# Kernel tuning notes

Hardware: AMD Instinct MI355X
Metric: run time of the kernel (lower is better)

Reference implementation:

```python
import jax, jax.numpy as jnp
import numpy as np

B, T_DIM, N, D, HID, NH = 2, 512, 6, 32, 128, 4
HD = HID // NH  # 32
GH = max(32, D)  # gater hidden = 32
FD = 128  # final_dim
EPS = 1e-5


def _ln(x, w, b):
    mu = jnp.mean(x, axis=-1, keepdims=True)
    var = jnp.var(x, axis=-1, keepdims=True)
    return (x - mu) * jax.lax.rsqrt(var + EPS) * w + b


def setup_inputs() -> dict:
    key = jax.random.key(0)
    ks = jax.random.split(key, 16)
    s_d = 1.0 / np.sqrt(D)
    s_h = 1.0 / np.sqrt(HID)
    s_g = 1.0 / np.sqrt(GH)
    return {
        "per_t_forces": jax.random.normal(ks[0], (B, T_DIM, N, D), jnp.float32),
        # gater: LayerNorm(D) -> Linear(D,GH) -> SiLU -> Linear(GH,1) (bias zero-init)
        "g_ln_w": jnp.ones((D,), jnp.float32),
        "g_ln_b": jnp.zeros((D,), jnp.float32),
        "g_w1": jax.random.uniform(ks[1], (D, GH), jnp.float32, -s_d, s_d),
        "g_b1": jax.random.uniform(ks[2], (GH,), jnp.float32, -s_d, s_d),
        "g_w2": jax.random.uniform(ks[3], (GH, 1), jnp.float32, -s_g, s_g),
        "g_b2": jnp.zeros((1,), jnp.float32),
        # QKV / out projections
        "q_w": jax.random.uniform(ks[4], (D, HID), jnp.float32, -s_d, s_d),
        "q_b": jax.random.uniform(ks[5], (HID,), jnp.float32, -s_d, s_d),
        "k_w": jax.random.uniform(ks[6], (D, HID), jnp.float32, -s_d, s_d),
        "k_b": jax.random.uniform(ks[7], (HID,), jnp.float32, -s_d, s_d),
        "v_w": jax.random.uniform(ks[8], (D, HID), jnp.float32, -s_d, s_d),
        "v_b": jax.random.uniform(ks[9], (HID,), jnp.float32, -s_d, s_d),
        "o_w": jax.random.uniform(ks[10], (HID, HID), jnp.float32, -s_h, s_h),
        "o_b": jax.random.uniform(ks[11], (HID,), jnp.float32, -s_h, s_h),
        # final: LayerNorm(HID) -> Linear(HID,FD) -> SiLU
        "f_ln_w": jnp.ones((HID,), jnp.float32),
        "f_ln_b": jnp.zeros((HID,), jnp.float32),
        "f_w": jax.random.uniform(ks[12], (HID, FD), jnp.float32, -s_h, s_h),
        "f_b": jax.random.uniform(ks[13], (FD,), jnp.float32, -s_h, s_h),
        "T": T_DIM,
    }


def reference(per_t_forces, g_ln_w, g_ln_b, g_w1, g_b1, g_w2, g_b2,
              q_w, q_b, k_w, k_b, v_w, v_b, o_w, o_b,
              f_ln_w, f_ln_b, f_w, f_b, T):
    b, tt, n, d = per_t_forces.shape
    L = T * n
    x = per_t_forces.reshape(b, L, d)

    # per-force learned gating
    h = jax.nn.silu(_ln(x, g_ln_w, g_ln_b) @ g_w1 + g_b1)
    gates = jax.nn.sigmoid((h @ g_w2 + g_b2)[..., 0])  # [B, L]
    g = gates[..., None]

    # gated QKV
    Q = (x @ q_w + q_b) * g
    K = (x @ k_w + k_b) * g
    V = (x @ v_w + v_b) * g

    Qh = Q.reshape(b, L, NH, HD)
    Kh = K.reshape(b, L, NH, HD)
    Vh = V.reshape(b, L, NH, HD)

    scale = 1.0 / np.sqrt(HD)
    scores = jnp.einsum("bihd,bjhd->bhij", Qh, Kh) * scale  # [B,NH,L,L]

    # block-causal over time: token j masked out if its time block > time of i
    t_idx = jnp.arange(L) // n
    mask = t_idx[None, :] > t_idx[:, None]  # [L, L], True = masked
    scores = jnp.where(mask[None, None], -jnp.inf, scores)

    A = jnp.maximum(jax.nn.softmax(scores, axis=-1), 1e-9)
    attn = jnp.einsum("bhij,bjhd->bihd", A, Vh).reshape(b, L, HID)

    out = attn @ o_w + o_b                     # [B, L, HID]
    per_t = out.reshape(b, T, n, HID).mean(axis=2)  # mean-pool over forces
    final = jax.nn.silu(_ln(per_t, f_ln_w, f_ln_b) @ f_w + f_b)  # [B, T, FD]
    return final
```

## Files before the change

kernel.cpp:

```cpp
#include <hip/hip_runtime.h>
#include <hip/hip_bf16.h>

#define BB   2
#define TT   512
#define NF   6
#define DD   32
#define HIDD 128
#define NHH  4
#define HDD  32
#define GHH  32
#define FDD  128
#define LL   (TT*NF)
#define EPSF 1e-5f
#define NQT16 (LL/16)

typedef __attribute__((ext_vector_type(8))) short  bf16x8;
typedef __attribute__((ext_vector_type(4))) float  f32x4;

#define MFMA16x16x32(a,b,c) __builtin_amdgcn_mfma_f32_16x16x32_bf16(a,b,c,0,0,0)

__device__ __forceinline__ unsigned short bfh(float f) {
    union { __hip_bfloat16 b; unsigned short u; } cv;
    cv.b = __float2bfloat16(f);
    return cv.u;
}
__device__ __forceinline__ float bff(unsigned short u) {
    return __uint_as_float(((unsigned)u) << 16);
}
__device__ __forceinline__ unsigned pk_bf16(float a, float b) {
    union { __hip_bfloat162 h2; unsigned u; } cv;
    cv.h2 = __float22bfloat162_rn(make_float2(a, b));
    return cv.u;
}
__device__ __forceinline__ bf16x8 ld8(const unsigned short* p) {
    return *reinterpret_cast<const bf16x8*>(p);
}

__device__ __forceinline__ float fexp2(float x) {
#if __has_builtin(__builtin_amdgcn_exp2f)
    return __builtin_amdgcn_exp2f(x);
#else
    return exp2f(x);
#endif
}

struct Frags {
    bf16x8 k0, k1;
    bf16x8 k2, k3;
    bf16x8 v0, v1, v2, v3;
};

__device__ __forceinline__ void load_tile(
    const unsigned short* __restrict__ Kh,
    const unsigned short* __restrict__ Vth,
    size_t hbT, int j0, int kloc0, int kloc1, int quad,
    size_t vb0, size_t vb1, Frags& f)
{
    const size_t kX0 = (hbT + j0 + kloc0) * HDD + quad * 8;
    const size_t kX1 = (hbT + j0 + kloc1) * HDD + quad * 8;
    f.k0 = ld8(Kh + kX0);
    f.k1 = ld8(Kh + kX1);
    f.k2 = ld8(Kh + kX0 + (size_t)32 * HDD);
    f.k3 = ld8(Kh + kX1 + (size_t)32 * HDD);
    const size_t vX = (size_t)j0 + quad * 8, vY = vX + 32;
    f.v0 = ld8(Vth + vb0 + vX);
    f.v1 = ld8(Vth + vb1 + vX);
    f.v2 = ld8(Vth + vb0 + vY);
    f.v3 = ld8(Vth + vb1 + vY);
}

__device__ __forceinline__ void compute_tile(
    const Frags& f, const bf16x8 qfh, const bf16x8 qfl,
    int j0, int jminw, int jend, int quad,
    float& m, float& l, f32x4& o0, f32x4& o1)
{
    const f32x4 z = {0.f, 0.f, 0.f, 0.f};
    f32x4 s0 = MFMA16x16x32(f.k0, qfh, z);
    f32x4 s1 = MFMA16x16x32(f.k1, qfh, z);
    f32x4 s2 = MFMA16x16x32(f.k2, qfh, z);
    f32x4 s3 = MFMA16x16x32(f.k3, qfh, z);
    s0 = MFMA16x16x32(f.k0, qfl, s0);
    s1 = MFMA16x16x32(f.k1, qfl, s1);
    s2 = MFMA16x16x32(f.k2, qfl, s2);
    s3 = MFMA16x16x32(f.k3, qfl, s3);

    float e[16], mx, ls, corr;
    if (j0 + 64 <= jminw) {
        f32x4 m4 = s0;
        #pragma unroll
        for (int r2 = 0; r2 < 4; r2++)
            m4[r2] = fmaxf(fmaxf(m4[r2], s1[r2]), fmaxf(s2[r2], s3[r2]));
        mx = fmaxf(fmaxf(m4[0], m4[1]), fmaxf(m4[2], m4[3]));
        mx = fmaxf(mx, __shfl_xor(mx, 16));
        mx = fmaxf(mx, __shfl_xor(mx, 32));
        mx = fmaxf(m, mx);
        corr = fexp2(m - mx); m = mx;
        ls = 0.f;
        #pragma unroll
        for (int r2 = 0; r2 < 4; r2++) {
            float e0 = fexp2(s0[r2] - mx);
            float e1 = fexp2(s1[r2] - mx);
            float e2 = fexp2(s2[r2] - mx);
            float e3 = fexp2(s3[r2] - mx);
            e[r2] = e0; e[4 + r2] = e1; e[8 + r2] = e2; e[12 + r2] = e3;
            ls += (e0 + e1) + (e2 + e3);
        }
    } else {
        const int je = jend - j0;
        const int k0 = 8 * quad;
        float t[16];
        #pragma unroll
        for (int r2 = 0; r2 < 4; r2++) {
            t[r2]      = (k0 + r2          < je) ? s0[r2] : -1e30f;
            t[4 + r2]  = (k0 + 4 + r2      < je) ? s1[r2] : -1e30f;
            t[8 + r2]  = (32 + k0 + r2     < je) ? s2[r2] : -1e30f;
            t[12 + r2] = (32 + k0 + 4 + r2 < je) ? s3[r2] : -1e30f;
        }
        mx = t[0];
        #pragma unroll
        for (int i = 1; i < 16; i++) mx = fmaxf(mx, t[i]);
        mx = fmaxf(mx, __shfl_xor(mx, 16));
        mx = fmaxf(mx, __shfl_xor(mx, 32));
        mx = fmaxf(m, mx);
        corr = fexp2(m - mx); m = mx;
        ls = 0.f;
        #pragma unroll
        for (int r2 = 0; r2 < 4; r2++) {
            float e0 = fexp2(t[r2] - mx);
            float e1 = fexp2(t[4 + r2] - mx);
            float e2 = fexp2(t[8 + r2] - mx);
            float e3 = fexp2(t[12 + r2] - mx);
            e0 = (k0 + r2          < je) ? e0 : 0.f;
            e1 = (k0 + 4 + r2      < je) ? e1 : 0.f;
            e2 = (32 + k0 + r2     < je) ? e2 : 0.f;
            e3 = (32 + k0 + 4 + r2 < je) ? e3 : 0.f;
            e[r2] = e0; e[4 + r2] = e1; e[8 + r2] = e2; e[12 + r2] = e3;
            ls += (e0 + e1) + (e2 + e3);
        }
    }
    l = l * corr + ls;
    #pragma unroll
    for (int i = 0; i < 4; i++) { o0[i] *= corr; o1[i] *= corr; }

    union { unsigned u[4]; bf16x8 v; } pbX, pbY;
    pbX.u[0] = pk_bf16(e[0],  e[1]);
    pbX.u[1] = pk_bf16(e[2],  e[3]);
    pbX.u[2] = pk_bf16(e[4],  e[5]);
    pbX.u[3] = pk_bf16(e[6],  e[7]);
    pbY.u[0] = pk_bf16(e[8],  e[9]);
    pbY.u[1] = pk_bf16(e[10], e[11]);
    pbY.u[2] = pk_bf16(e[12], e[13]);
    pbY.u[3] = pk_bf16(e[14], e[15]);

    o0 = MFMA16x16x32(f.v0, pbX.v, o0);
    o1 = MFMA16x16x32(f.v1, pbX.v, o1);
    o0 = MFMA16x16x32(f.v2, pbY.v, o0);
    o1 = MFMA16x16x32(f.v3, pbY.v, o1);
}

__global__ __launch_bounds__(128) void gate_qkv_kernel(
    const float* __restrict__ x,
    const float* __restrict__ g_ln_w, const float* __restrict__ g_ln_b,
    const float* __restrict__ g_w1,   const float* __restrict__ g_b1,
    const float* __restrict__ g_w2,   const float* __restrict__ g_b2,
    const float* __restrict__ q_w,    const float* __restrict__ q_b,
    const float* __restrict__ k_w,    const float* __restrict__ k_b,
    const float* __restrict__ v_w,    const float* __restrict__ v_b,
    unsigned short* __restrict__ Qh, unsigned short* __restrict__ Ql,
    unsigned short* __restrict__ Kh,
    unsigned short* __restrict__ Vth)
{
    const int tok0 = blockIdx.x * 4;
    const int tid  = threadIdx.x;

    __shared__ float xs[4][DD];
    __shared__ float lns[4][DD];
    __shared__ float hs[4][GHH];
    __shared__ float gate_s[4];

    xs[tid >> 5][tid & 31] = x[(size_t)tok0 * DD + tid];
    __syncthreads();

    const int tk = (tid >> 5) & 1;
    const int d5 = tid & 31;
    if (tid < 64) {
        #pragma unroll
        for (int tt = 0; tt < 2; tt++) {
            int t = tt * 2 + tk;
            float xv = xs[t][d5];
            float s1 = xv, s2 = xv * xv;
            #pragma unroll
            for (int m = 16; m >= 1; m >>= 1) {
                s1 += __shfl_xor(s1, m, 32);
                s2 += __shfl_xor(s2, m, 32);
            }
            float mu  = s1 * (1.0f / DD);
            float var = s2 * (1.0f / DD) - mu * mu;
            float r   = rsqrtf(var + EPSF);
            lns[t][d5] = (xv - mu) * r * g_ln_w[d5] + g_ln_b[d5];
        }
    }
    __syncthreads();
    if (tid < 64) {
        #pragma unroll
        for (int tt = 0; tt < 2; tt++) {
            int t = tt * 2 + tk;
            float acc = g_b1[d5];
            #pragma unroll
            for (int d = 0; d < DD; d++) acc += lns[t][d] * g_w1[d * GHH + d5];
            hs[t][d5] = acc / (1.0f + __expf(-acc));
        }
    }
    __syncthreads();
    if (tid < 64) {
        #pragma unroll
        for (int tt = 0; tt < 2; tt++) {
            int t = tt * 2 + tk;
            float p = hs[t][d5] * g_w2[d5];
            #pragma unroll
            for (int m = 16; m >= 1; m >>= 1) p += __shfl_xor(p, m, 32);
            if (d5 == 0) gate_s[t] = 1.0f / (1.0f + __expf(-(p + g_b2[0])));
        }
    }
    __syncthreads();

    const int col = tid;
    float aq[4], ak[4], av[4];
    #pragma unroll
    for (int t = 0; t < 4; t++) { aq[t] = q_b[col]; ak[t] = k_b[col]; av[t] = v_b[col]; }
    #pragma unroll
    for (int d = 0; d < DD; d++) {
        float wq = q_w[d * HIDD + col];
        float wk = k_w[d * HIDD + col];
        float wv = v_w[d * HIDD + col];
        #pragma unroll
        for (int t = 0; t < 4; t++) {
            float xd = xs[t][d];
            aq[t] += xd * wq; ak[t] += xd * wk; av[t] += xd * wv;
        }
    }

    const int b    = tok0 / LL;
    const int l0   = tok0 - b * LL;
    const int head = col >> 5;
    const int d5c  = col & 31;
    const float scale = 0.25503486f;

    unsigned short vh[4];
    #pragma unroll
    for (int t = 0; t < 4; t++) {
        const float g = gate_s[t];
        const size_t a = ((size_t)(b * NHH + head) * LL + l0 + t) * HDD + d5c;
        float qv = aq[t] * g * scale;
        unsigned short h = bfh(qv); Qh[a] = h; Ql[a] = bfh(qv - bff(h));
        Kh[a] = bfh(ak[t] * g);
        vh[t] = bfh(av[t] * g);
    }
    const size_t vbase = ((size_t)(b * NHH + head) * HDD + d5c) * LL + l0;
    *(ushort4*)(Vth + vbase) = make_ushort4(vh[0], vh[1], vh[2], vh[3]);
}

__global__ __launch_bounds__(256) void attn_mfma(
    const unsigned short* __restrict__ Qh, const unsigned short* __restrict__ Ql,
    const unsigned short* __restrict__ Kh,
    const unsigned short* __restrict__ Vth,
    float* __restrict__ P, int C, int NCH)
{
    const int lin = blockIdx.x;
    const int bh  = lin & 7;
    const int jj  = lin >> 3;
    const int ch  = jj / (LL / 64);
    const int qt  = (LL / 64 - 1) - (jj % (LL / 64));
    const int j0c = C * ch;
    const int jmax_blk = ((qt * 64 + 63) / NF + 1) * NF;
    if (j0c >= jmax_blk) return;

    const int tid  = threadIdx.x;
    const int w    = tid >> 6;
    const int lane = tid & 63;
    const int rr   = lane & 15;
    const int quad = lane >> 4;

    const int ig0   = qt * 64 + w * 16;
    const int ig    = ig0 + rr;
    const int jend  = (ig / NF + 1) * NF;
    const int jmaxw = ((ig0 + 15) / NF + 1) * NF;
    const int jminw = (ig0 / NF + 1) * NF;

    const int kend = min(jmaxw - j0c, C);
    if (kend <= 0) return;

    const size_t hbT = (size_t)bh * LL;
    const size_t qo  = (hbT + ig) * HDD + quad * 8;
    const bf16x8 qfh = ld8(Qh + qo);
    const bf16x8 qfl = ld8(Ql + qo);

    const int kloc0 = 8 * (rr >> 2) + (rr & 3);
    const int kloc1 = kloc0 + 4;

    const size_t vb0 = ((size_t)bh * HDD + rr)      * LL;
    const size_t vb1 = ((size_t)bh * HDD + rr + 16) * LL;

    f32x4 oA0 = {0.f,0.f,0.f,0.f}, oA1 = {0.f,0.f,0.f,0.f};
    f32x4 oB0 = {0.f,0.f,0.f,0.f}, oB1 = {0.f,0.f,0.f,0.f};
    f32x4 oC0 = {0.f,0.f,0.f,0.f}, oC1 = {0.f,0.f,0.f,0.f};
    float mA = -1e30f, lA = 0.f, mB = -1e30f, lB = 0.f, mC = -1e30f, lC = 0.f;

    const int ntile = (kend + 63) >> 6;

    for (int i = 0; i < ntile; i += 3) {
        const int  j0A  = j0c + (i << 6);
        const bool hasB = (i + 1 < ntile);
        const bool hasC = (i + 2 < ntile);
        const int  j0B  = j0c + ((hasB ? i + 1 : i) << 6);
        const int  j0C  = j0c + ((hasC ? i + 2 : i) << 6);

        Frags fA, fB, fC;
        load_tile(Kh, Vth, hbT, j0A, kloc0, kloc1, quad, vb0, vb1, fA);
        load_tile(Kh, Vth, hbT, j0B, kloc0, kloc1, quad, vb0, vb1, fB);
        load_tile(Kh, Vth, hbT, j0C, kloc0, kloc1, quad, vb0, vb1, fC);

        compute_tile(fA, qfh, qfl, j0A, jminw, jend, quad, mA, lA, oA0, oA1);
        if (hasB)
            compute_tile(fB, qfh, qfl, j0B, jminw, jend, quad, mB, lB, oB0, oB1);
        if (hasC)
            compute_tile(fC, qfh, qfl, j0C, jminw, jend, quad, mC, lC, oC0, oC1);
    }

    const float mm = fmaxf(mA, fmaxf(mB, mC));
    const float wa = fexp2(mA - mm), wb = fexp2(mB - mm), wc = fexp2(mC - mm);
    float l = lA * wa + lB * wb + lC * wc;
    f32x4 o0, o1;
    #pragma unroll
    for (int i = 0; i < 4; i++) {
        o0[i] = oA0[i] * wa + oB0[i] * wb + oC0[i] * wc;
        o1[i] = oA1[i] * wa + oB1[i] * wb + oC1[i] * wc;
    }

    l += __shfl_xor(l, 16);
    l += __shfl_xor(l, 32);

    float* dst = P + ((((size_t)bh * NQT16 + (ig0 >> 4)) * NCH + ch) * 16 + rr) * 36;
    *(f32x4*)(dst + quad * 4)      = o0;
    *(f32x4*)(dst + 16 + quad * 4) = o1;
    if (quad == 0) { dst[32] = mm; dst[33] = l; }
}

__global__ __launch_bounds__(128) void final_kernel(
    const float* __restrict__ P,
    const float* __restrict__ o_w,    const float* __restrict__ o_b,
    const float* __restrict__ f_ln_w, const float* __restrict__ f_ln_b,
    const float* __restrict__ f_w,    const float* __restrict__ f_b,
    float* __restrict__ out, int C, int NCH)
{
    const int t = blockIdx.x;
    const int b = blockIdx.y;
    const int d = threadIdx.x;
    const int h  = d >> 5;
    const int hd = d & 31;
    const int bh = b * NHH + h;

    __shared__ float ms[HIDD];
    __shared__ float lnbuf[HIDD];
    __shared__ float w1[2], w2[2];

    const int jmax = (t + 1) * NF;
    const int nch  = min(NCH, (jmax + C - 1) / C);

    float M[NF], L[NF], O[NF];
    #pragma unroll
    for (int f = 0; f < NF; f++) { M[f] = -1e30f; L[f] = 0.f; O[f] = 0.f; }

    for (int c = 0; c < nch; c++) {
        #pragma unroll
        for (int f = 0; f < NF; f++) {
            const int row = t * NF + f;
            const float* pr = P + ((((size_t)bh * NQT16 + (row >> 4)) * NCH + c)
                                   * 16 + (row & 15)) * 36;
            const float mc = pr[32], lc = pr[33], oc = pr[hd];
            const float mm = fmaxf(M[f], mc);
            const float sa = fexp2(M[f] - mm), sb = fexp2(mc - mm);
            O[f] = O[f] * sa + oc * sb;
            L[f] = L[f] * sa + lc * sb;
            M[f] = mm;
        }
    }
    float acc = 0.0f;
    #pragma unroll
    for (int f = 0; f < NF; f++) acc += O[f] / L[f];
    acc *= (1.0f / NF);
    ms[d] = acc;
    __syncthreads();

    float ov = o_b[d];
    for (int k = 0; k < HIDD; k++) ov += ms[k] * o_w[k * HIDD + d];

    float s1 = ov, s2 = ov * ov;
    #pragma unroll
    for (int m = 32; m >= 1; m >>= 1) { s1 += __shfl_xor(s1, m); s2 += __shfl_xor(s2, m); }
    if ((d & 63) == 0) { w1[d >> 6] = s1; w2[d >> 6] = s2; }
    __syncthreads();
    float S1 = w1[0] + w1[1], S2 = w2[0] + w2[1];
    float mu  = S1 * (1.0f / HIDD);
    float var = S2 * (1.0f / HIDD) - mu * mu;
    float r   = rsqrtf(var + EPSF);
    float lnv = (ov - mu) * r * f_ln_w[d] + f_ln_b[d];
    lnbuf[d] = lnv;
    __syncthreads();

    float fv = f_b[d];
    for (int k = 0; k < HIDD; k++) fv += lnbuf[k] * f_w[k * HIDD + d];
    fv = fv / (1.0f + __expf(-fv));

    out[((size_t)(b * TT + t)) * FDD + d] = fv;
}

extern "C" void kernel_launch(void* const* d_in, const int* in_sizes, int n_in,
                              void* d_out, int out_size, void* d_ws, size_t ws_size,
                              hipStream_t stream)
{
    const float* x      = (const float*)d_in[0];
    const float* g_ln_w = (const float*)d_in[1];
    const float* g_ln_b = (const float*)d_in[2];
    const float* g_w1   = (const float*)d_in[3];
    const float* g_b1   = (const float*)d_in[4];
    const float* g_w2   = (const float*)d_in[5];
    const float* g_b2   = (const float*)d_in[6];
    const float* q_w    = (const float*)d_in[7];
    const float* q_b    = (const float*)d_in[8];
    const float* k_w    = (const float*)d_in[9];
    const float* k_b    = (const float*)d_in[10];
    const float* v_w    = (const float*)d_in[11];
    const float* v_b    = (const float*)d_in[12];
    const float* o_w    = (const float*)d_in[13];
    const float* o_b    = (const float*)d_in[14];
    const float* f_ln_w = (const float*)d_in[15];
    const float* f_ln_b = (const float*)d_in[16];
    const float* f_w    = (const float*)d_in[17];
    const float* f_b    = (const float*)d_in[18];

    const size_t ntok = (size_t)BB * NHH * LL * HDD;
    unsigned short* Qh  = (unsigned short*)d_ws;
    unsigned short* Ql  = Qh  + ntok;
    unsigned short* Kh  = Ql  + ntok;
    unsigned short* Vth = Kh + 2 * ntok;
    float* Pw = (float*)(Vth + 2 * ntok);

    const long long bf_floats = (long long)(6 * ntok) / 2;
    const long long unit = 8LL * NQT16 * 16 * 36;
    long long avail = (long long)(ws_size / 4) - bf_floats - 4096;
    int NCH = (int)(avail / unit);
    if (NCH > 16) NCH = 16;
    if (NCH < 1) NCH = 1;
    const int C = 64 * ((LL + 64 * NCH - 1) / (64 * NCH));

    gate_qkv_kernel<<<(BB * LL) / 4, 128, 0, stream>>>(
        x, g_ln_w, g_ln_b, g_w1, g_b1, g_w2, g_b2,
        q_w, q_b, k_w, k_b, v_w, v_b, Qh, Ql, Kh, Vth);

    attn_mfma<<<(LL / 64) * NCH * BB * NHH, 256, 0, stream>>>(
        Qh, Ql, Kh, Vth, Pw, C, NCH);

    final_kernel<<<dim3(TT, BB), 128, 0, stream>>>(
        Pw, o_w, o_b, f_ln_w, f_ln_b, f_w, f_b, (float*)d_out, C, NCH);
}
```

Measured before the change: 160.3 us.

## Stage K/V chunk in LDS and fix chunk count to eight

Each attention block now cooperatively copies its 384-key chunk of K and transposed V into shared memory (with row padding on V), then the four waves read MFMA fragments from LDS instead of global memory. The three-way independent online-softmax streams are replaced by a single stream with one-tile software prefetch from LDS. The chunk count is now hard-coded to 8 instead of being derived from workspace size. This cuts redundant global/L2 traffic across waves, at the cost of a barrier, about 48KB of LDS per block (lower occupancy), and less ILP in the softmax loop.

```diff
diff --git a/kernel.cpp b/kernel.cpp
--- a/kernel.cpp
+++ b/kernel.cpp
@@ -14,6 +14,10 @@
 #define EPSF 1e-5f
 #define NQT16 (LL/16)
 
+#define NCHC 8
+#define CCH  384
+#define VPAD 8
+
 typedef __attribute__((ext_vector_type(8))) short  bf16x8;
 typedef __attribute__((ext_vector_type(4))) float  f32x4;
 
@@ -50,23 +54,22 @@
     bf16x8 v0, v1, v2, v3;
 };
 
-__device__ __forceinline__ void load_tile(
-    const unsigned short* __restrict__ Kh,
-    const unsigned short* __restrict__ Vth,
-    size_t hbT, int j0, int kloc0, int kloc1, int quad,
-    size_t vb0, size_t vb1, Frags& f)
-{
-    const size_t kX0 = (hbT + j0 + kloc0) * HDD + quad * 8;
-    const size_t kX1 = (hbT + j0 + kloc1) * HDD + quad * 8;
-    f.k0 = ld8(Kh + kX0);
-    f.k1 = ld8(Kh + kX1);
-    f.k2 = ld8(Kh + kX0 + (size_t)32 * HDD);
-    f.k3 = ld8(Kh + kX1 + (size_t)32 * HDD);
-    const size_t vX = (size_t)j0 + quad * 8, vY = vX + 32;
-    f.v0 = ld8(Vth + vb0 + vX);
-    f.v1 = ld8(Vth + vb1 + vX);
-    f.v2 = ld8(Vth + vb0 + vY);
-    f.v3 = ld8(Vth + vb1 + vY);
+__device__ __forceinline__ void load_tile_lds(
+    const unsigned short* ldsK, const unsigned short* ldsV,
+    int j0loc, int kloc0, int kloc1, int quad, int rr, Frags& f)
+{
+    const int kX0 = (j0loc + kloc0) * HDD + quad * 8;
+    const int kX1 = (j0loc + kloc1) * HDD + quad * 8;
+    f.k0 = ld8(ldsK + kX0);
+    f.k1 = ld8(ldsK + kX1);
+    f.k2 = ld8(ldsK + kX0 + 32 * HDD);
+    f.k3 = ld8(ldsK + kX1 + 32 * HDD);
+    const int vX = j0loc + quad * 8, vY = vX + 32;
+    const int vr0 = rr * (CCH + VPAD), vr1 = (rr + 16) * (CCH + VPAD);
+    f.v0 = ld8(ldsV + vr0 + vX);
+    f.v1 = ld8(ldsV + vr1 + vX);
+    f.v2 = ld8(ldsV + vr0 + vY);
+    f.v3 = ld8(ldsV + vr1 + vY);
 }
 
 __device__ __forceinline__ void compute_tile(
@@ -264,18 +267,38 @@
     const unsigned short* __restrict__ Qh, const unsigned short* __restrict__ Ql,
     const unsigned short* __restrict__ Kh,
     const unsigned short* __restrict__ Vth,
-    float* __restrict__ P, int C, int NCH)
+    float* __restrict__ P)
 {
     const int lin = blockIdx.x;
     const int bh  = lin & 7;
     const int jj  = lin >> 3;
     const int ch  = jj / (LL / 64);
     const int qt  = (LL / 64 - 1) - (jj % (LL / 64));
-    const int j0c = C * ch;
+    const int j0c = CCH * ch;
     const int jmax_blk = ((qt * 64 + 63) / NF + 1) * NF;
     if (j0c >= jmax_blk) return;
 
-    const int tid  = threadIdx.x;
+    __shared__ __align__(16) unsigned short ldsK[CCH * HDD];
+    __shared__ __align__(16) unsigned short ldsV[HDD * (CCH + VPAD)];
+
+    const int tid = threadIdx.x;
+
+    {
+        const unsigned short* gK = Kh + ((size_t)bh * LL + j0c) * HDD;
+        const unsigned short* gV = Vth + (size_t)bh * HDD * LL + j0c;
+        const int r  = tid >> 3;
+        const int c8 = tid & 7;
+        #pragma unroll
+        for (int it = 0; it < CCH / 64; it++) {
+            const int uk = it * 256 + tid;
+            *reinterpret_cast<bf16x8*>(&ldsK[uk * 8]) = ld8(gK + uk * 8);
+            const int off = it * 64 + c8 * 8;
+            *reinterpret_cast<bf16x8*>(&ldsV[r * (CCH + VPAD) + off]) =
+                ld8(gV + (size_t)r * LL + off);
+        }
+    }
+    __syncthreads();
+
     const int w    = tid >> 6;
     const int lane = tid & 63;
     const int rr   = lane & 15;
@@ -287,63 +310,42 @@
     const int jmaxw = ((ig0 + 15) / NF + 1) * NF;
     const int jminw = (ig0 / NF + 1) * NF;
 
-    const int kend = min(jmaxw - j0c, C);
+    const int kend = min(jmaxw - j0c, CCH);
     if (kend <= 0) return;
 
-    const size_t hbT = (size_t)bh * LL;
-    const size_t qo  = (hbT + ig) * HDD + quad * 8;
+    const size_t qo = ((size_t)bh * LL + ig) * HDD + quad * 8;
     const bf16x8 qfh = ld8(Qh + qo);
     const bf16x8 qfl = ld8(Ql + qo);
 
     const int kloc0 = 8 * (rr >> 2) + (rr & 3);
     const int kloc1 = kloc0 + 4;
 
-    const size_t vb0 = ((size_t)bh * HDD + rr)      * LL;
-    const size_t vb1 = ((size_t)bh * HDD + rr + 16) * LL;
-
-    f32x4 oA0 = {0.f,0.f,0.f,0.f}, oA1 = {0.f,0.f,0.f,0.f};
-    f32x4 oB0 = {0.f,0.f,0.f,0.f}, oB1 = {0.f,0.f,0.f,0.f};
-    f32x4 oC0 = {0.f,0.f,0.f,0.f}, oC1 = {0.f,0.f,0.f,0.f};
-    float mA = -1e30f, lA = 0.f, mB = -1e30f, lB = 0.f, mC = -1e30f, lC = 0.f;
+    f32x4 o0 = {0.f,0.f,0.f,0.f}, o1 = {0.f,0.f,0.f,0.f};
+    float m = -1e30f, l = 0.f;
 
     const int ntile = (kend + 63) >> 6;
 
-    for (int i = 0; i < ntile; i += 3) {
-        const int  j0A  = j0c + (i << 6);
-        const bool hasB = (i + 1 < ntile);
-        const bool hasC = (i + 2 < ntile);
-        const int  j0B  = j0c + ((hasB ? i + 1 : i) << 6);
-        const int  j0C  = j0c + ((hasC ? i + 2 : i) << 6);
-
-        Frags fA, fB, fC;
-        load_tile(Kh, Vth, hbT, j0A, kloc0, kloc1, quad, vb0, vb1, fA);
-        load_tile(Kh, Vth, hbT, j0B, kloc0, kloc1, quad, vb0, vb1, fB);
-        load_tile(Kh, Vth, hbT, j0C, kloc0, kloc1, quad, vb0, vb1, fC);
-
-        compute_tile(fA, qfh, qfl, j0A, jminw, jend, quad, mA, lA, oA0, oA1);
-        if (hasB)
-            compute_tile(fB, qfh, qfl, j0B, jminw, jend, quad, mB, lB, oB0, oB1);
-        if (hasC)
-            compute_tile(fC, qfh, qfl, j0C, jminw, jend, quad, mC, lC, oC0, oC1);
-    }
-
-    const float mm = fmaxf(mA, fmaxf(mB, mC));
-    const float wa = fexp2(mA - mm), wb = fexp2(mB - mm), wc = fexp2(mC - mm);
-    float l = lA * wa + lB * wb + lC * wc;
-    f32x4 o0, o1;
-    #pragma unroll
-    for (int i = 0; i < 4; i++) {
-        o0[i] = oA0[i] * wa + oB0[i] * wb + oC0[i] * wc;
-        o1[i] = oA1[i] * wa + oB1[i] * wb + oC1[i] * wc;
+    Frags f0;
+    load_tile_lds(ldsK, ldsV, 0, kloc0, kloc1, quad, rr, f0);
+    for (int i = 0; i < ntile; i++) {
+        const int j0 = j0c + (i << 6);
+        if (i + 1 < ntile) {
+            Frags f1;
+            load_tile_lds(ldsK, ldsV, (i + 1) << 6, kloc0, kloc1, quad, rr, f1);
+            compute_tile(f0, qfh, qfl, j0, jminw, jend, quad, m, l, o0, o1);
+            f0 = f1;
+        } else {
+            compute_tile(f0, qfh, qfl, j0, jminw, jend, quad, m, l, o0, o1);
+        }
     }
 
     l += __shfl_xor(l, 16);
     l += __shfl_xor(l, 32);
 
-    float* dst = P + ((((size_t)bh * NQT16 + (ig0 >> 4)) * NCH + ch) * 16 + rr) * 36;
+    float* dst = P + ((((size_t)bh * NQT16 + (ig0 >> 4)) * NCHC + ch) * 16 + rr) * 36;
     *(f32x4*)(dst + quad * 4)      = o0;
     *(f32x4*)(dst + 16 + quad * 4) = o1;
-    if (quad == 0) { dst[32] = mm; dst[33] = l; }
+    if (quad == 0) { dst[32] = m; dst[33] = l; }
 }
 
 __global__ __launch_bounds__(128) void final_kernel(
@@ -446,21 +448,13 @@
     unsigned short* Vth = Kh + 2 * ntok;
     float* Pw = (float*)(Vth + 2 * ntok);
 
-    const long long bf_floats = (long long)(6 * ntok) / 2;
-    const long long unit = 8LL * NQT16 * 16 * 36;
-    long long avail = (long long)(ws_size / 4) - bf_floats - 4096;
-    int NCH = (int)(avail / unit);
-    if (NCH > 16) NCH = 16;
-    if (NCH < 1) NCH = 1;
-    const int C = 64 * ((LL + 64 * NCH - 1) / (64 * NCH));
-
     gate_qkv_kernel<<<(BB * LL) / 4, 128, 0, stream>>>(
         x, g_ln_w, g_ln_b, g_w1, g_b1, g_w2, g_b2,
         q_w, q_b, k_w, k_b, v_w, v_b, Qh, Ql, Kh, Vth);
 
-    attn_mfma<<<(LL / 64) * NCH * BB * NHH, 256, 0, stream>>>(
-        Qh, Ql, Kh, Vth, Pw, C, NCH);
+    attn_mfma<<<(LL / 64) * NCHC * BB * NHH, 256, 0, stream>>>(
+        Qh, Ql, Kh, Vth, Pw);
 
     final_kernel<<<dim3(TT, BB), 128, 0, stream>>>(
-        Pw, o_w, o_b, f_ln_w, f_ln_b, f_w, f_b, (float*)d_out, C, NCH);
-}
+        Pw, o_w, o_b, f_ln_w, f_ln_b, f_w, f_b, (float*)d_out, CCH, NCHC);
+}
```

After: 140.4 us. 1.14x faster.
